# Kernel tuning notes

Measured on AMD Instinct MI355X. Metric: run time of the kernel, lower is better.

The kernel has to match this reference:

```python
import jax, jax.numpy as jnp
import numpy as np

TOPK = 13
NUM_CLASSES = 80
ALPHA = 1.0
BETA = 3.0
EPS = 1e-9
K_NEAR = 4
N_BINS = 36  # theta bins: arange(0, 360, 10)


def _dist_max_per_bin(anc_points, gt_pts):
    """gt_pts: (bs,nm,360,2), anc_points: (na,2) -> (bs,nm,na,36) ray targets."""
    d = gt_pts[:, :, None, :, :] - anc_points[None, None, :, None, :]  # (bs,nm,na,360,2)
    dist = jnp.sqrt(jnp.sum(d * d, axis=-1))                           # (bs,nm,na,360)
    ang = jnp.rad2deg(jnp.arctan2(d[..., 1], d[..., 0])) % 360.0       # (bs,nm,na,360)
    theta = jnp.arange(0, 360, 360 // N_BINS).astype(ang.dtype)        # (36,)

    def per_theta(th):
        diff = jnp.abs(ang - th)
        diff = jnp.where(diff > 180.0, 360.0 - diff, diff)
        neg_v, idx = jax.lax.top_k(-diff, K_NEAR)   # 4 nearest-angle contour pts
        val = -neg_v
        dk = jnp.take_along_axis(dist, idx, axis=-1)
        dk = jnp.where(jnp.min(val, axis=-1, keepdims=True) > 3.0, 1e-6, dk)
        return jnp.max(dk, axis=-1)                 # (bs,nm,na)

    dm = jax.lax.map(per_theta, theta)              # (36,bs,nm,na); chunked to bound memory
    return jnp.maximum(jnp.moveaxis(dm, 0, -1), 1e-6)


def _mask_iou(target, pred):
    l_max = jnp.maximum(target, pred)
    l_min = jnp.maximum(jnp.minimum(target, pred), 1e-6)
    return jnp.sum(l_min, -1) / jnp.sum(l_max, -1)


def _forward(pd_scores, pd_bboxes, anc_points, gt_labels, gt_bboxes, mask_gt, gt_coor):
    bs, na, nc = pd_scores.shape
    nm = gt_bboxes.shape[1]
    gl = gt_labels[..., 0]            # (bs,nm) int
    mgt = mask_gt[..., 0]             # (bs,nm) float
    gt_pts = gt_coor.reshape(bs, nm, 360, 2)

    # select_candidates_in_gts: anchor center strictly inside gt box
    lt, rb = gt_bboxes[..., :2], gt_bboxes[..., 2:]
    deltas = jnp.concatenate([anc_points[None, None] - lt[:, :, None],
                              rb[:, :, None] - anc_points[None, None]], axis=-1)
    mask_in_gts = (jnp.min(deltas, -1) > 1e-9).astype(pd_scores.dtype)  # (bs,nm,na)
    mask_sel = (mask_in_gts * mgt[:, :, None]) > 0

    # get_box_metrics_polar (dense over (bs,nm,na) instead of boolean-mask select)
    dist_max = _dist_max_per_bin(anc_points, gt_pts)                    # (bs,nm,na,36)
    overlaps = jnp.where(mask_sel, _mask_iou(dist_max, pd_bboxes[:, None]), 0.0)
    bbox_scores = jnp.take_along_axis(jnp.swapaxes(pd_scores, 1, 2), gl[:, :, None], axis=1)
    bbox_scores = jnp.where(mask_sel, bbox_scores, 0.0)
    align_metric = (bbox_scores ** ALPHA) * (overlaps ** BETA)

    # select_topk_candidates
    _, topk_idxs = jax.lax.top_k(align_metric, TOPK)
    topk_idxs = jnp.where(mgt[:, :, None] > 0, topk_idxs, 0)
    count = jnp.sum(jax.nn.one_hot(topk_idxs, na, dtype=align_metric.dtype), axis=-2)
    mask_topk = jnp.where(count > 1, 0.0, count)
    mask_pos = mask_topk * mask_in_gts * mgt[:, :, None]

    # select_highest_overlaps
    fg = jnp.sum(mask_pos, -2)                                          # (bs,na)
    multi = fg[:, None, :] > 1
    is_max = jnp.moveaxis(jax.nn.one_hot(jnp.argmax(overlaps, 1), nm, dtype=mask_pos.dtype), -1, 1)
    mask_pos = jnp.where(multi, is_max, mask_pos)
    fg_mask = jnp.sum(mask_pos, -2)
    target_gt_idx = jnp.argmax(mask_pos, -2)                            # (bs,na)

    # per-positive ray-distance targets + polar centerness (dense, masked)
    mask_pos_b = mask_pos > 0
    gt_dist = jnp.where(mask_pos_b[..., None], dist_max, 0.0)           # (bs,nm,na,36)
    cent = jnp.sqrt(jnp.min(dist_max, -1) / jnp.max(dist_max, -1))
    centerness_gt = jnp.where(mask_pos_b, cent, 0.0)                    # (bs,nm,na)

    # get_targets
    target_labels = jnp.maximum(jnp.take_along_axis(gl, target_gt_idx, axis=1), 0)
    target_bboxes = jnp.take_along_axis(gt_bboxes, target_gt_idx[..., None], axis=1)
    target_scores = jax.nn.one_hot(target_labels, NUM_CLASSES, dtype=pd_scores.dtype)
    target_scores = jnp.where((fg_mask > 0)[..., None], target_scores, 0.0)

    am = align_metric * mask_pos
    pos_align = jnp.max(am, -1, keepdims=True)
    pos_ov = jnp.max(overlaps * mask_pos, -1, keepdims=True)
    norm_align = jnp.max(am * pos_ov / (pos_align + EPS), -2)[..., None]  # (bs,na,1)
    target_scores = target_scores * norm_align

    return (target_labels, target_bboxes, target_scores, mask_pos_b,
            target_gt_idx, gt_dist, centerness_gt, fg_mask > 0)


def setup_inputs():
    key = jax.random.key(0)
    k = jax.random.split(key, 6)
    bs, nc, nm = 2, 80, 10
    pts, strs = [], []
    for s in (8, 16, 32):  # 640x640 YOLO grid -> 8400 anchors
        n = 640 // s
        yv, xv = np.meshgrid(np.arange(n), np.arange(n), indexing='ij')
        pts.append(np.stack([(xv + 0.5) * s, (yv + 0.5) * s], -1).reshape(-1, 2))
        strs.append(np.full((pts[-1].shape[0], 1), s, dtype=np.float32))
    anc_points = jnp.asarray(np.concatenate(pts).astype(np.float32))
    stride_tensor = jnp.asarray(np.concatenate(strs))
    na = anc_points.shape[0]
    pd_scores = jax.random.uniform(k[0], (bs, na, nc), dtype=jnp.float32)
    pd_bboxes = jax.random.uniform(k[1], (bs, na, 36), dtype=jnp.float32) * 100.0 + 1.0
    gt_labels = jax.random.randint(k[2], (bs, nm, 1), 0, nc)
    ctr = jax.random.uniform(k[3], (bs, nm, 2), dtype=jnp.float32) * 440.0 + 100.0
    wh = jax.random.uniform(k[4], (bs, nm, 2), dtype=jnp.float32) * 140.0 + 40.0
    gt_bboxes = jnp.concatenate([ctr - wh / 2.0, ctr + wh / 2.0], -1)
    th = jnp.arange(360.0) * (jnp.pi / 180.0)
    rad = (jnp.min(wh, -1, keepdims=True) / 2.0) * (0.6 + 0.4 * jax.random.uniform(k[5], (bs, nm, 360), dtype=jnp.float32))
    ray = jnp.stack([jnp.cos(th), jnp.sin(th)], -1)  # (360,2)
    gt_coor = (ctr[:, :, None, :] + rad[..., None] * ray[None, None]).reshape(bs, nm, 720)
    mask_gt = jnp.ones((bs, nm, 1), dtype=jnp.float32).at[1, 7:].set(0.0)
    return dict(pd_scores=pd_scores, pd_bboxes=pd_bboxes, anc_points=anc_points,
                gt_labels=gt_labels, gt_bboxes=gt_bboxes, mask_gt=mask_gt,
                gt_coor=gt_coor, stride_tensor=stride_tensor, ss=640,
                gt_center=ctr, imgsz=640)


def reference(pd_scores, pd_bboxes, anc_points, gt_labels, gt_bboxes, mask_gt, gt_coor, stride_tensor, ss, gt_center, imgsz):
    # ss, gt_center, imgsz, stride_tensor are accepted (as in the torch signature) but unused
    return _forward(pd_scores, pd_bboxes, anc_points, gt_labels, gt_bboxes, mask_gt, gt_coor)
```

## Files before the change

### kernel.cpp

```cpp
#include <hip/hip_runtime.h>

#define BS 2
#define NM 10
#define NA 8400
#define NC 80
#define NBIN 36
#define KTOP 13
#define NRECT (BS*NM*3)
#define WDIST_CAP 16384

__device__ __forceinline__ void rect_one(int bm, int lv,
    const float* __restrict__ gtb, const float* __restrict__ mgt,
    int& x0, int& y0, int& cx, int& cy, int& cnt, int& n, int& base){
  cnt = 0; x0 = 0; y0 = 0; cx = 0; cy = 0; n = 0; base = 0;
  if (mgt[bm] > 0.f){
    float s = (float)(8 << lv);
    n = 640 >> (3 + lv);
    base = (lv == 0) ? 0 : ((lv == 1) ? 6400 : 8000);
    float lx = gtb[bm*4+0], ly = gtb[bm*4+1];
    float rx = gtb[bm*4+2], ry = gtb[bm*4+3];
    int a0 = (int)ceilf(lx/s - 0.5f); a0 = min(max(a0, 0), n);
    while (a0 > 0   &&  (((a0-1)+0.5f)*s - lx > 1e-9f)) a0--;
    while (a0 < n   && !(((a0  )+0.5f)*s - lx > 1e-9f)) a0++;
    int a1 = (int)floorf(rx/s - 0.5f); a1 = min(max(a1, -1), n-1);
    while (a1 < n-1 &&  (rx - ((a1+1)+0.5f)*s > 1e-9f)) a1++;
    while (a1 >= 0  && !(rx - ((a1  )+0.5f)*s > 1e-9f)) a1--;
    int b0 = (int)ceilf(ly/s - 0.5f); b0 = min(max(b0, 0), n);
    while (b0 > 0   &&  (((b0-1)+0.5f)*s - ly > 1e-9f)) b0--;
    while (b0 < n   && !(((b0  )+0.5f)*s - ly > 1e-9f)) b0++;
    int b1 = (int)floorf(ry/s - 0.5f); b1 = min(max(b1, -1), n-1);
    while (b1 < n-1 &&  (ry - ((b1+1)+0.5f)*s > 1e-9f)) b1++;
    while (b1 >= 0  && !(ry - ((b1  )+0.5f)*s > 1e-9f)) b1--;
    cx = max(0, a1 - a0 + 1);
    cy = max(0, b1 - b0 + 1);
    cnt = cx * cy;
    x0 = a0; y0 = b0;
  }
}

__device__ __forceinline__ void rect_setup(int tid,
    const float* __restrict__ gtb, const float* __restrict__ mgt,
    int* sx0, int* sy0, int* scx, int* scy, int* scum, int* sn, int* sbase){
  if (tid < NRECT){
    int bm = tid/3, lv = tid - bm*3;
    int x0, y0, cx, cy, cnt, n, base;
    rect_one(bm, lv, gtb, mgt, x0, y0, cx, cy, cnt, n, base);
    sx0[tid] = x0; sy0[tid] = y0; scx[tid] = cx; scy[tid] = cy;
    scum[tid] = cnt; sn[tid] = n; sbase[tid] = base;
  }
  __syncthreads();
  if (tid == 0){
    int acc = 0;
    for (int r = 0; r < NRECT; r++){ int c = scum[r]; scum[r] = acc; acc += c; }
    scum[NRECT] = acc;
  }
  __syncthreads();
}

__device__ __forceinline__ int pair_from_p(int p,
    const int* sx0, const int* sy0, const int* scx,
    const int* scum, const int* sn, const int* sbase){
  int r = 0;
  while (r < NRECT-1 && scum[r+1] <= p) r++;
  int idx = p - scum[r];
  int cx = scx[r];
  int yi = idx / cx;
  int xi = idx - yi*cx;
  int a = sbase[r] + (sy0[r] + yi)*sn[r] + (sx0[r] + xi);
  int bm = r/3;
  return bm*NA + a;
}

__global__ __launch_bounds__(256)
void k_dist(const float* __restrict__ pds, const float* __restrict__ pdb,
            const float* __restrict__ anc, const int* __restrict__ gl,
            const float* __restrict__ gtb, const float* __restrict__ mgt,
            const float* __restrict__ coor,
            float* __restrict__ out, float* __restrict__ wf){
  float* o_labels  = out;
  float* o_bboxes  = o_labels + BS*NA;
  float* o_scores  = o_bboxes + BS*NA*4;
  float* o_maskpos = o_scores + (size_t)BS*NA*NC;
  float* o_gtidx   = o_maskpos + BS*NM*NA;
  float* o_gtdist  = o_gtidx + BS*NA;
  float* o_cent    = o_gtdist + (size_t)BS*NM*NA*NBIN;
  float* o_fg      = o_cent + BS*NM*NA;

  float* w_align = wf + 16;
  float* w_ovl   = w_align + BS*NM*NA;
  float* w_dist  = w_ovl + BS*NM*NA;

  __shared__ int sx0[NRECT], sy0[NRECT], scx[NRECT], scy[NRECT], scum[NRECT+1], sn[NRECT], sbase[NRECT];
  __shared__ float2 s_da[360];
  __shared__ float  s_m[NBIN*49];

  int tid = threadIdx.x;
  int lane = tid & 63, wave = tid >> 6;

  rect_setup(tid, gtb, mgt, sx0, sy0, scx, scy, scum, sn, sbase);
  int total = scum[NRECT];

  {
    int gtid = blockIdx.x*256 + tid, gsz = gridDim.x*256;
    float4 z4 = make_float4(0.f,0.f,0.f,0.f);
    float4* zs = (float4*)o_scores;
    for (int i = gtid; i < (BS*NA*NC)/4; i += gsz) zs[i] = z4;
    float4* zg = (float4*)o_gtdist;
    for (int i = gtid; i < (BS*NM*NA*NBIN)/4; i += gsz) zg[i] = z4;
    float4* zc = (float4*)o_cent;
    for (int i = gtid; i < (BS*NM*NA)/4; i += gsz) zc[i] = z4;
    float4* zm = (float4*)o_maskpos;
    for (int i = gtid; i < (BS*NM*NA)/4; i += gsz) zm[i] = z4;
    if (gtid < 16) wf[gtid] = 0.f;
    for (int t = gtid; t < BS*NA; t += gsz){
      int b = t / NA;
      o_gtidx[t] = 0.f;
      o_fg[t] = 0.f;
      int lbl = gl[b*NM]; if (lbl < 0) lbl = 0;
      o_labels[t] = (float)lbl;
      const float* bx = gtb + (b*NM)*4;
      ((float4*)o_bboxes)[t] = make_float4(bx[0], bx[1], bx[2], bx[3]);
    }
    for (int row = gtid; row < BS*NM*NA; row += gsz){
      int bm = row / NA;
      int a  = row - bm*NA;
      int lv = (a < 6400) ? 0 : ((a < 8000) ? 1 : 2);
      int ai = a - ((lv == 0) ? 0 : ((lv == 1) ? 6400 : 8000));
      int r = bm*3 + lv;
      bool inrect = false;
      if (scx[r] > 0 && scy[r] > 0){
        int n = sn[r];
        int y = ai / n, x = ai - y*n;
        inrect = (x >= sx0[r] && x < sx0[r]+scx[r] &&
                  y >= sy0[r] && y < sy0[r]+scy[r]);
      }
      if (!inrect) w_ovl[row] = 0.f;
    }
  }

  int id = tid;
  int bin = id % 36;
  int chunk = id / 36;
  bool act = (id < 216);
  float th = (float)(bin*10);

  for (int p = blockIdx.x; p < total; p += gridDim.x){
    int t = pair_from_p(p, sx0, sy0, scx, scum, sn, sbase);
    int a = t % NA; int bm = t / NA; int b = bm / NM;
    float ax = anc[2*a], ay = anc[2*a+1];
    const float* cc = coor + bm*720;
    for (int i = tid; i < 360; i += 256){
      float dx = cc[2*i]   - ax;
      float dy = cc[2*i+1] - ay;
      float dist = sqrtf(dx*dx + dy*dy);
      float an = atan2f(dy, dx) * 57.29577951308232f;
      if (an < 0.f) an += 360.f;
      s_da[i] = make_float2(dist, an);
    }
    __syncthreads();
    if (act){
      float v0=1e30f, v1=1e30f, v2=1e30f, v3=1e30f;
      float d0=0.f, d1=0.f, d2=0.f, d3=0.f;
      int base = chunk*60;
      for (int k = 0; k < 60; k++){
        float2 da = s_da[base + k];
        float diff = fabsf(da.y - th);
        diff = fminf(diff, 360.f - diff);
        if (diff < v3){
          v3 = diff; d3 = da.x;
          if (v3 < v2){ float tv=v2; v2=v3; v3=tv; float td=d2; d2=d3; d3=td; }
          if (v2 < v1){ float tv=v1; v1=v2; v2=tv; float td=d1; d1=d2; d2=td; }
          if (v1 < v0){ float tv=v0; v0=v1; v1=tv; float td=d0; d0=d1; d1=td; }
        }
      }
      int mb = bin*49 + chunk*8;
      s_m[mb+0]=v0; s_m[mb+1]=v1; s_m[mb+2]=v2; s_m[mb+3]=v3;
      s_m[mb+4]=d0; s_m[mb+5]=d1; s_m[mb+6]=d2; s_m[mb+7]=d3;
    }
    __syncthreads();
    if (wave == 0){
      float sum_min = 0.f, sum_max = 0.f;
      if (lane < NBIN){
        int mb = lane*49;
        float h0=s_m[mb+0], h1=s_m[mb+8],  h2=s_m[mb+16],
              h3=s_m[mb+24], h4=s_m[mb+32], h5=s_m[mb+40];
        int p0=0, p1=0, p2=0, p3=0, p4=0, p5=0;
        float v0m = 0.f, dmax = 0.f;
#pragma unroll
        for (int step = 0; step < 4; step++){
          float bv = h0; int bw = 0;
          if (h1 < bv){ bv = h1; bw = 1; }
          if (h2 < bv){ bv = h2; bw = 2; }
          if (h3 < bv){ bv = h3; bw = 3; }
          if (h4 < bv){ bv = h4; bw = 4; }
          if (h5 < bv){ bv = h5; bw = 5; }
          float dd;
          if (bw == 0){ dd = s_m[mb+ 4+p0]; p0++; h0 = (p0<4)? s_m[mb   +p0] : 1e30f; }
          else if (bw == 1){ dd = s_m[mb+12+p1]; p1++; h1 = (p1<4)? s_m[mb+ 8+p1] : 1e30f; }
          else if (bw == 2){ dd = s_m[mb+20+p2]; p2++; h2 = (p2<4)? s_m[mb+16+p2] : 1e30f; }
          else if (bw == 3){ dd = s_m[mb+28+p3]; p3++; h3 = (p3<4)? s_m[mb+24+p3] : 1e30f; }
          else if (bw == 4){ dd = s_m[mb+36+p4]; p4++; h4 = (p4<4)? s_m[mb+32+p4] : 1e30f; }
          else             { dd = s_m[mb+44+p5]; p5++; h5 = (p5<4)? s_m[mb+40+p5] : 1e30f; }
          if (step == 0) v0m = bv;
          dmax = fmaxf(dmax, dd);
        }
        float dm = (v0m > 3.0f) ? 1e-6f : dmax;
        float dfin = fmaxf(dm, 1e-6f);
        if (p < WDIST_CAP) w_dist[(size_t)p*NBIN + lane] = dfin;
        float pr = pdb[((size_t)b*NA + a)*NBIN + lane];
        sum_max = fmaxf(dfin, pr);
        sum_min = fmaxf(fminf(dfin, pr), 1e-6f);
      }
      for (int off = 32; off > 0; off >>= 1){
        sum_min += __shfl_down(sum_min, off);
        sum_max += __shfl_down(sum_max, off);
      }
      if (lane == 0){
        float ov = sum_min / sum_max;
        int cls = gl[bm];
        float sc = pds[((size_t)b*NA + a)*NC + cls];
        w_align[t] = sc * ov * ov * ov;
        w_ovl[t]   = ov;
      }
    }
    __syncthreads();
  }
}

__global__ __launch_bounds__(256)
void k_tail(const float* __restrict__ gtb, const float* __restrict__ mgt,
            const float* __restrict__ w_align, const float* __restrict__ w_ovl,
            const float* __restrict__ w_dist, const int* __restrict__ gl,
            float* __restrict__ o_labels, float* __restrict__ o_bboxes,
            float* __restrict__ o_maskpos, float* __restrict__ o_gtidx,
            float* __restrict__ o_fg,
            float* __restrict__ o_gtdist, float* __restrict__ o_cent,
            float* __restrict__ o_scores,
            int* __restrict__ w_sel, int* __restrict__ done){
  __shared__ int sx0[NRECT], sy0[NRECT], scx[NRECT], scy[NRECT], scum[NRECT+1], sn[NRECT], sbase[NRECT];
  __shared__ float sv[256*KTOP];
  __shared__ int   si[256*KTOP];
  __shared__ float wv4[4];
  __shared__ int   wi4[4];
  __shared__ int   sel[BS*NM*KTOP];
  __shared__ unsigned paB[BS*NM], poB[BS*NM];
  __shared__ int fcnt;
  __shared__ int   fT[BS*NM*KTOP];
  __shared__ int   fA[BS*NM*KTOP];
  __shared__ int   fL[BS*NM*KTOP];
  __shared__ float fV[BS*NM*KTOP];
  __shared__ int sLast;

  int tid = threadIdx.x;
  int lane = tid & 63, wave = tid >> 6;

  rect_setup(tid, gtb, mgt, sx0, sy0, scx, scy, scum, sn, sbase);

  int bm = blockIdx.x;
  {
    const float* al = w_align + (size_t)bm*NA;
    int pbase = scum[bm*3], pm1 = scum[bm*3+1], pm2 = scum[bm*3+2], pend = scum[bm*3+3];

    float v[KTOP]; int ix[KTOP];
#pragma unroll
    for (int j = 0; j < KTOP; j++){ v[j] = -1.f; ix[j] = 0x7fffffff; }
    for (int p = pbase + tid; p < pend; p += 256){
      int r = bm*3 + ((p >= pm1) + (p >= pm2));
      int idx = p - scum[r];
      int cx = scx[r];
      int yi = idx / cx;
      int xi = idx - yi*cx;
      int a = sbase[r] + (sy0[r] + yi)*sn[r] + (sx0[r] + xi);
      float x = al[a];
      if (x > v[KTOP-1]){
        v[KTOP-1] = x; ix[KTOP-1] = a;
#pragma unroll
        for (int j = KTOP-1; j > 0; j--){
          if (v[j] > v[j-1]){
            float tv = v[j-1]; v[j-1] = v[j]; v[j] = tv;
            int   ti = ix[j-1]; ix[j-1] = ix[j]; ix[j] = ti;
          }
        }
      }
    }
#pragma unroll
    for (int j = 0; j < KTOP; j++){ sv[tid*KTOP+j] = v[j]; si[tid*KTOP+j] = ix[j]; }

    int head = 0;
    for (int r = 0; r < KTOP; r++){
      float cv = sv[tid*KTOP + head];
      int   ci = si[tid*KTOP + head];
      float rv = cv; int ri = ci;
      for (int off = 32; off > 0; off >>= 1){
        float ov = __shfl_down(rv, off);
        int   oi = __shfl_down(ri, off);
        if (ov > rv || (ov == rv && oi < ri)){ rv = ov; ri = oi; }
      }
      if (lane == 0){ wv4[wave] = rv; wi4[wave] = ri; }
      __syncthreads();
      float Wv = wv4[0]; int Wi = wi4[0];
#pragma unroll
      for (int w = 1; w < 4; w++){
        float ov = wv4[w]; int oi = wi4[w];
        if (ov > Wv || (ov == Wv && oi < Wi)){ Wv = ov; Wi = oi; }
      }
      if (ci == Wi && head < KTOP-1) head++;
      if (tid == 0)
        __hip_atomic_store(&w_sel[bm*KTOP + r], (Wv > 0.f) ? Wi : -1,
                           __ATOMIC_RELAXED, __HIP_MEMORY_SCOPE_AGENT);
      __syncthreads();
    }
  }

  if (tid == 0){
    __threadfence();
    int old = __hip_atomic_fetch_add(done, 1, __ATOMIC_ACQ_REL, __HIP_MEMORY_SCOPE_AGENT);
    sLast = (old == BS*NM - 1) ? 1 : 0;
  }
  __syncthreads();
  if (!sLast) return;

  for (int s = tid; s < BS*NM*KTOP; s += 256)
    sel[s] = __hip_atomic_load(&w_sel[s], __ATOMIC_RELAXED, __HIP_MEMORY_SCOPE_AGENT);
  if (tid < BS*NM){ paB[tid] = 0u; poB[tid] = 0u; }
  if (tid == 0) fcnt = 0;
  __syncthreads();

  for (int s = tid; s < BS*NM*KTOP; s += 256){
    int a = sel[s];
    if (a >= 0){
      int sbm = s / KTOP;
      int b   = sbm / NM;
      int s0 = b*NM*KTOP;
      int cnt = 0, minS = 1 << 30;
      for (int s2 = s0; s2 < s0 + NM*KTOP; s2++){
        if (sel[s2] == a){ cnt++; if (s2 < minS) minS = s2; }
      }
      if (s == minS){
        int bi = sbm - b*NM;
        if (cnt > 1){
          float bv = -1.f; bi = 0;
#pragma unroll
          for (int mm = 0; mm < NM; mm++){
            float vv = w_ovl[((size_t)(b*NM+mm))*NA + a];
            if (vv > bv){ bv = vv; bi = mm; }
          }
        }
        int bmw = b*NM + bi;
        int ta  = b*NA + a;
        o_maskpos[(size_t)bmw*NA + a] = 1.f;
        o_gtidx[ta] = (float)bi;
        o_fg[ta] = 1.f;
        int lbl = gl[bmw]; if (lbl < 0) lbl = 0;
        o_labels[ta] = (float)lbl;
        const float* bx = gtb + bmw*4;
        ((float4*)o_bboxes)[ta] = make_float4(bx[0], bx[1], bx[2], bx[3]);
        float av  = w_align[(size_t)bmw*NA + a];
        float ovv = w_ovl[(size_t)bmw*NA + a];
        atomicMax(&paB[bmw], __float_as_uint(av));
        atomicMax(&poB[bmw], __float_as_uint(ovv));
        int j = atomicAdd(&fcnt, 1);
        fT[j] = bmw*NA + a; fA[j] = ta; fL[j] = lbl; fV[j] = av;
      }
    }
  }
  __syncthreads();

  int nf = fcnt;
  for (int j = tid; j < nf; j += 256){
    int tf = fT[j];
    int a = tf % NA; int bmw = tf / NA;
    int lv = (a < 6400) ? 0 : ((a < 8000) ? 1 : 2);
    int ai = a - ((lv == 0) ? 0 : ((lv == 1) ? 6400 : 8000));
    int r = bmw*3 + lv;
    int n = sn[r];
    int y = ai / n, x = ai - y*n;
    int p = scum[r] + (y - sy0[r])*scx[r] + (x - sx0[r]);
    const float4* src = (const float4*)(w_dist + (size_t)p*NBIN);
    float4* dst = (float4*)(o_gtdist + (size_t)tf*NBIN);
    float vmin = 1e30f, vmax = 0.f;
#pragma unroll
    for (int q = 0; q < 9; q++){
      float4 v4 = src[q];
      dst[q] = v4;
      vmin = fminf(vmin, fminf(fminf(v4.x, v4.y), fminf(v4.z, v4.w)));
      vmax = fmaxf(vmax, fmaxf(fmaxf(v4.x, v4.y), fmaxf(v4.z, v4.w)));
    }
    o_cent[tf] = sqrtf(vmin / vmax);
    float paf = __uint_as_float(paB[bmw]);
    float pof = __uint_as_float(poB[bmw]);
    o_scores[(size_t)fA[j]*NC + fL[j]] = fV[j] * pof / (paf + 1e-9f);
  }
}

extern "C" void kernel_launch(void* const* d_in, const int* in_sizes, int n_in,
                              void* d_out, int out_size, void* d_ws, size_t ws_size,
                              hipStream_t stream){
  const float* pds  = (const float*)d_in[0];
  const float* pdb  = (const float*)d_in[1];
  const float* anc  = (const float*)d_in[2];
  const int*   gl   = (const int*)  d_in[3];
  const float* gtb  = (const float*)d_in[4];
  const float* mgt  = (const float*)d_in[5];
  const float* coor = (const float*)d_in[6];

  float* out = (float*)d_out;
  float* o_labels  = out;
  float* o_bboxes  = o_labels + BS*NA;
  float* o_scores  = o_bboxes + BS*NA*4;
  float* o_maskpos = o_scores + (size_t)BS*NA*NC;
  float* o_gtidx   = o_maskpos + BS*NM*NA;
  float* o_gtdist  = o_gtidx + BS*NA;
  float* o_cent    = o_gtdist + (size_t)BS*NM*NA*NBIN;
  float* o_fg      = o_cent + BS*NM*NA;

  float* wf      = (float*)d_ws;
  int*   done    = (int*)d_ws;
  float* w_align = wf + 16;
  float* w_ovl   = w_align + BS*NM*NA;
  float* w_dist  = w_ovl + BS*NM*NA;
  int*   w_sel   = (int*)(w_dist + (size_t)WDIST_CAP*NBIN);

  k_dist<<<4096, 256, 0, stream>>>(pds, pdb, anc, gl, gtb, mgt, coor, out, wf);
  k_tail<<<BS*NM, 256, 0, stream>>>(gtb, mgt, w_align, w_ovl, w_dist, gl,
                                    o_labels, o_bboxes, o_maskpos, o_gtidx, o_fg,
                                    o_gtdist, o_cent, o_scores, w_sel, done);
}
```

Baseline: 160.9 us.

## Bucket contour points by angle and search only neighboring bins for top-4

Replaces the brute-force per-bin scan of all 360 contour points with a counting sort into 10-degree buckets, so each theta bin searches only its three neighboring buckets, with a full-scan wave fallback when the 4th-nearest angle exceeds the bucketed window. Keys pack the angle difference with the point index to keep tie-breaking deterministic. The rectangle lookup becomes a binary search. This cuts the per-pair comparison work but adds extra barriers, shared atomics and a divergent fallback path.

```diff
diff --git a/kernel.cpp b/kernel.cpp
--- a/kernel.cpp
+++ b/kernel.cpp
@@ -8,6 +8,8 @@
 #define KTOP 13
 #define NRECT (BS*NM*3)
 #define WDIST_CAP 16384
+
+typedef unsigned long long ull;
 
 __device__ __forceinline__ void rect_one(int bm, int lv,
     const float* __restrict__ gtb, const float* __restrict__ mgt,
@@ -60,8 +62,9 @@
 __device__ __forceinline__ int pair_from_p(int p,
     const int* sx0, const int* sy0, const int* scx,
     const int* scum, const int* sn, const int* sbase){
-  int r = 0;
-  while (r < NRECT-1 && scum[r+1] <= p) r++;
+  int lo = 0, hi = NRECT - 1;
+  while (lo < hi){ int mid = (lo + hi + 1) >> 1; if (scum[mid] <= p) lo = mid; else hi = mid - 1; }
+  int r = lo;
   int idx = p - scum[r];
   int cx = scx[r];
   int yi = idx / cx;
@@ -69,6 +72,12 @@
   int a = sbase[r] + (sy0[r] + yi)*sn[r] + (sx0[r] + xi);
   int bm = r/3;
   return bm*NA + a;
+}
+
+__device__ __forceinline__ ull shflx_u64(ull v, int off){
+  unsigned lo = (unsigned)v, hi = (unsigned)(v >> 32);
+  lo = __shfl_xor(lo, off); hi = __shfl_xor(hi, off);
+  return ((ull)hi << 32) | lo;
 }
 
 __global__ __launch_bounds__(256)
@@ -91,8 +100,17 @@
   float* w_dist  = w_ovl + BS*NM*NA;
 
   __shared__ int sx0[NRECT], sy0[NRECT], scx[NRECT], scy[NRECT], scum[NRECT+1], sn[NRECT], sbase[NRECT];
-  __shared__ float2 s_da[360];
-  __shared__ float  s_m[NBIN*49];
+  __shared__ float2 s_ad[360];
+  __shared__ unsigned short s_ix[360];
+  __shared__ int s_cnt[NBIN], s_off[NBIN+1], s_cur[NBIN];
+  __shared__ ull  s_k[NBIN*29];
+  __shared__ float s_d[NBIN*29];
+  __shared__ float s_res[NBIN];
+  __shared__ int s_fbl[NBIN];
+  __shared__ int s_nfb;
+
+  float2* s_tmp = (float2*)s_k;
+  unsigned char* s_bu = ((unsigned char*)s_k) + 2880;
 
   int tid = threadIdx.x;
   int lane = tid & 63, wave = tid >> 6;
@@ -138,74 +156,160 @@
     }
   }
 
-  int id = tid;
-  int bin = id % 36;
-  int chunk = id / 36;
-  bool act = (id < 216);
-  float th = (float)(bin*10);
+  if (tid < NBIN) s_cnt[tid] = 0;
+  if (tid == 0) s_nfb = 0;
+  __syncthreads();
+
+  int bin7 = tid % 36;
+  int slot7 = tid / 36;
 
   for (int p = blockIdx.x; p < total; p += gridDim.x){
     int t = pair_from_p(p, sx0, sy0, scx, scum, sn, sbase);
     int a = t % NA; int bm = t / NA; int b = bm / NM;
     float ax = anc[2*a], ay = anc[2*a+1];
     const float* cc = coor + bm*720;
+
     for (int i = tid; i < 360; i += 256){
       float dx = cc[2*i]   - ax;
       float dy = cc[2*i+1] - ay;
       float dist = sqrtf(dx*dx + dy*dy);
       float an = atan2f(dy, dx) * 57.29577951308232f;
       if (an < 0.f) an += 360.f;
-      s_da[i] = make_float2(dist, an);
-    }
-    __syncthreads();
-    if (act){
-      float v0=1e30f, v1=1e30f, v2=1e30f, v3=1e30f;
-      float d0=0.f, d1=0.f, d2=0.f, d3=0.f;
-      int base = chunk*60;
-      for (int k = 0; k < 60; k++){
-        float2 da = s_da[base + k];
-        float diff = fabsf(da.y - th);
-        diff = fminf(diff, 360.f - diff);
-        if (diff < v3){
-          v3 = diff; d3 = da.x;
-          if (v3 < v2){ float tv=v2; v2=v3; v3=tv; float td=d2; d2=d3; d3=td; }
-          if (v2 < v1){ float tv=v1; v1=v2; v2=tv; float td=d1; d1=d2; d2=td; }
-          if (v1 < v0){ float tv=v0; v0=v1; v1=tv; float td=d0; d0=d1; d1=td; }
+      int bu = (int)(an * 0.1f); bu = min(bu, NBIN-1);
+      s_tmp[i] = make_float2(an, dist);
+      s_bu[i] = (unsigned char)bu;
+      atomicAdd(&s_cnt[bu], 1);
+    }
+    __syncthreads();
+    if (wave == 0){
+      int c = (lane < NBIN) ? s_cnt[lane] : 0;
+      int incl = c;
+#pragma unroll
+      for (int st = 1; st < 64; st <<= 1){
+        int o = __shfl_up(incl, st);
+        if (lane >= st) incl += o;
+      }
+      if (lane < NBIN){ s_off[lane+1] = incl; s_cur[lane] = incl - c; }
+      if (lane == 0) s_off[0] = 0;
+    }
+    __syncthreads();
+    for (int i = tid; i < 360; i += 256){
+      int bu = s_bu[i];
+      float2 ad = s_tmp[i];
+      int pos = atomicAdd(&s_cur[bu], 1);
+      s_ad[pos] = ad;
+      s_ix[pos] = (unsigned short)i;
+    }
+    __syncthreads();
+
+#define EVALJ(J, TH) { \
+      float2 ad = s_ad[J]; \
+      unsigned int ixv = s_ix[J]; \
+      float df = fabsf(ad.x - (TH)); \
+      df = fminf(df, 360.f - df); \
+      ull key = ((ull)__float_as_uint(df) << 32) | ixv; \
+      if (key < k3){ \
+        k3 = key; d3 = ad.y; \
+        if (k3 < k2){ ull tk=k2; k2=k3; k3=tk; float td=d2; d2=d3; d3=td; } \
+        if (k2 < k1){ ull tk=k1; k1=k2; k2=tk; float td=d1; d1=d2; d2=td; } \
+        if (k1 < k0){ ull tk=k0; k0=k1; k1=tk; float td=d0; d0=d1; d1=td; } \
+      } }
+
+    if (slot7 < 7){
+      float th = (float)(bin7*10);
+      int r0s, r0e, r1s, r1e;
+      if (bin7 == 0)      { r0s = s_off[35]; r0e = s_off[36]; r1s = 0; r1e = s_off[2]; }
+      else if (bin7 == 35){ r0s = s_off[34]; r0e = s_off[36]; r1s = 0; r1e = s_off[1]; }
+      else                { r0s = s_off[bin7-1]; r0e = s_off[bin7+2]; r1s = 0; r1e = 0; }
+      int L0 = r0e - r0s, L = L0 + (r1e - r1s);
+      ull k0,k1,k2,k3; float d0,d1,d2,d3;
+      k0=k1=k2=k3=~0ull; d0=d1=d2=d3=0.f;
+      for (int w = slot7; w < L; w += 7){
+        int j = (w < L0) ? (r0s + w) : (r1s + w - L0);
+        EVALJ(j, th)
+      }
+      int mb = bin7*29 + slot7*4;
+      s_k[mb+0]=k0; s_k[mb+1]=k1; s_k[mb+2]=k2; s_k[mb+3]=k3;
+      s_d[mb+0]=d0; s_d[mb+1]=d1; s_d[mb+2]=d2; s_d[mb+3]=d3;
+    }
+    __syncthreads();
+
+    if (wave == 0 && lane < NBIN){
+      int mb = lane*29;
+      ull h0=s_k[mb+0], h1=s_k[mb+4],  h2=s_k[mb+8],  h3=s_k[mb+12],
+          h4=s_k[mb+16], h5=s_k[mb+20], h6=s_k[mb+24];
+      int p0=0,p1=0,p2=0,p3=0,p4=0,p5=0,p6=0;
+      float v0m = 0.f, d4v = 0.f, dmax = 0.f;
+#pragma unroll
+      for (int step = 0; step < 4; step++){
+        ull bk = h0; int bw = 0;
+        if (h1 < bk){ bk = h1; bw = 1; }
+        if (h2 < bk){ bk = h2; bw = 2; }
+        if (h3 < bk){ bk = h3; bw = 3; }
+        if (h4 < bk){ bk = h4; bw = 4; }
+        if (h5 < bk){ bk = h5; bw = 5; }
+        if (h6 < bk){ bk = h6; bw = 6; }
+        float dd;
+        if (bw == 0){ dd = s_d[mb   +p0]; p0++; h0 = (p0<4)? s_k[mb   +p0] : ~0ull; }
+        else if (bw == 1){ dd = s_d[mb+ 4+p1]; p1++; h1 = (p1<4)? s_k[mb+ 4+p1] : ~0ull; }
+        else if (bw == 2){ dd = s_d[mb+ 8+p2]; p2++; h2 = (p2<4)? s_k[mb+ 8+p2] : ~0ull; }
+        else if (bw == 3){ dd = s_d[mb+12+p3]; p3++; h3 = (p3<4)? s_k[mb+12+p3] : ~0ull; }
+        else if (bw == 4){ dd = s_d[mb+16+p4]; p4++; h4 = (p4<4)? s_k[mb+16+p4] : ~0ull; }
+        else if (bw == 5){ dd = s_d[mb+20+p5]; p5++; h5 = (p5<4)? s_k[mb+20+p5] : ~0ull; }
+        else             { dd = s_d[mb+24+p6]; p6++; h6 = (p6<4)? s_k[mb+24+p6] : ~0ull; }
+        if (step == 0) v0m = __uint_as_float((unsigned)(bk >> 32));
+        if (step == 3) d4v = __uint_as_float((unsigned)(bk >> 32));
+        dmax = fmaxf(dmax, dd);
+      }
+      if (!(v0m <= 3.0f)){
+        s_res[lane] = 1e-6f;
+      } else if (!(d4v <= 9.99f)){
+        int fi = atomicAdd(&s_nfb, 1);
+        s_fbl[fi] = lane;
+      } else {
+        s_res[lane] = fmaxf(dmax, 1e-6f);
+      }
+    }
+    __syncthreads();
+
+    int nfb = s_nfb;
+    if (nfb > 0){
+      for (int f = wave; f < nfb; f += 4){
+        int fb = s_fbl[f];
+        float th = (float)(fb*10);
+        ull k0,k1,k2,k3; float d0,d1,d2,d3;
+        k0=k1=k2=k3=~0ull; d0=d1=d2=d3=0.f;
+        for (int j = lane; j < 360; j += 64){
+          EVALJ(j, th)
         }
-      }
-      int mb = bin*49 + chunk*8;
-      s_m[mb+0]=v0; s_m[mb+1]=v1; s_m[mb+2]=v2; s_m[mb+3]=v3;
-      s_m[mb+4]=d0; s_m[mb+5]=d1; s_m[mb+6]=d2; s_m[mb+7]=d3;
-    }
-    __syncthreads();
+        ull hk = k0; float hd = d0; int hp = 0;
+        float dmax = 0.f;
+#pragma unroll
+        for (int r = 0; r < 4; r++){
+          ull mk = hk; float md = hd;
+#pragma unroll
+          for (int off = 1; off < 64; off <<= 1){
+            ull ok = shflx_u64(mk, off);
+            float od = __shfl_xor(md, off);
+            if (ok < mk){ mk = ok; md = od; }
+          }
+          if (hk == mk){
+            hp++;
+            hk = (hp==1)? k1 : (hp==2)? k2 : (hp==3)? k3 : ~0ull;
+            hd = (hp==1)? d1 : (hp==2)? d2 : (hp==3)? d3 : 0.f;
+          }
+          dmax = fmaxf(dmax, md);
+        }
+        if (lane == 0) s_res[fb] = fmaxf(dmax, 1e-6f);
+      }
+    }
+    __syncthreads();
+#undef EVALJ
+
     if (wave == 0){
       float sum_min = 0.f, sum_max = 0.f;
       if (lane < NBIN){
-        int mb = lane*49;
-        float h0=s_m[mb+0], h1=s_m[mb+8],  h2=s_m[mb+16],
-              h3=s_m[mb+24], h4=s_m[mb+32], h5=s_m[mb+40];
-        int p0=0, p1=0, p2=0, p3=0, p4=0, p5=0;
-        float v0m = 0.f, dmax = 0.f;
-#pragma unroll
-        for (int step = 0; step < 4; step++){
-          float bv = h0; int bw = 0;
-          if (h1 < bv){ bv = h1; bw = 1; }
-          if (h2 < bv){ bv = h2; bw = 2; }
-          if (h3 < bv){ bv = h3; bw = 3; }
-          if (h4 < bv){ bv = h4; bw = 4; }
-          if (h5 < bv){ bv = h5; bw = 5; }
-          float dd;
-          if (bw == 0){ dd = s_m[mb+ 4+p0]; p0++; h0 = (p0<4)? s_m[mb   +p0] : 1e30f; }
-          else if (bw == 1){ dd = s_m[mb+12+p1]; p1++; h1 = (p1<4)? s_m[mb+ 8+p1] : 1e30f; }
-          else if (bw == 2){ dd = s_m[mb+20+p2]; p2++; h2 = (p2<4)? s_m[mb+16+p2] : 1e30f; }
-          else if (bw == 3){ dd = s_m[mb+28+p3]; p3++; h3 = (p3<4)? s_m[mb+24+p3] : 1e30f; }
-          else if (bw == 4){ dd = s_m[mb+36+p4]; p4++; h4 = (p4<4)? s_m[mb+32+p4] : 1e30f; }
-          else             { dd = s_m[mb+44+p5]; p5++; h5 = (p5<4)? s_m[mb+40+p5] : 1e30f; }
-          if (step == 0) v0m = bv;
-          dmax = fmaxf(dmax, dd);
-        }
-        float dm = (v0m > 3.0f) ? 1e-6f : dmax;
-        float dfin = fmaxf(dm, 1e-6f);
+        float dfin = s_res[lane];
         if (p < WDIST_CAP) w_dist[(size_t)p*NBIN + lane] = dfin;
         float pr = pdb[((size_t)b*NA + a)*NBIN + lane];
         sum_max = fmaxf(dfin, pr);
@@ -223,6 +327,8 @@
         w_ovl[t]   = ov;
       }
     }
+    if (tid < NBIN) s_cnt[tid] = 0;
+    if (tid == 0) s_nfb = 0;
     __syncthreads();
   }
 }
```

Result: no change. 158.1 us (-1.7%).
